# Kernel optimization log

Measured on AMD Instinct MI355X. Metric: run time of the kernel, lower is better.

## Reference

```python
import jax, jax.numpy as jnp
import numpy as np
import math

MODES = 32
IN_CH = 32
OUT_CH = 32
SIZE = 2048
BATCH = 8
FILTER_STRENGTH = 4.0
MAX_AMP = 1.0
AMP_SHARP = 1.0
POLE_OFF_SCALE = 0.1
POLE_MIN = 0.1
POLE_MAX = 100.0
CAUSAL_SAFETY = 1.0


def setup_inputs() -> dict:
    key = jax.random.key(0)
    ks = jax.random.split(key, 6)
    # polar-amp init matching the torch module
    fan_in = MODES * IN_CH
    target_amp = math.sqrt(2.0 / fan_in)
    target_sig = max(0.01, min(0.99, target_amp / MAX_AMP))
    init_bias = math.log(target_sig / (1.0 - target_sig)) / AMP_SHARP
    init_scale = 1.0 / math.sqrt(IN_CH * OUT_CH * MODES)
    return {
        "x": jax.random.normal(ks[0], (BATCH, IN_CH, SIZE), jnp.float32),
        "c_star": jax.random.uniform(ks[1], (BATCH,), jnp.float32),
        "dt_star": jnp.full((1,), 0.5, jnp.float32),
        "dx_star": jnp.full((1,), 1.0 / SIZE, jnp.float32),
        "weight_log_amp": init_bias + jax.random.normal(ks[2], (MODES, IN_CH, OUT_CH), jnp.float32) * init_scale,
        "weight_phase": jax.random.normal(ks[3], (MODES, IN_CH, OUT_CH), jnp.float32),
        "log_poles": jnp.linspace(math.log(1.0), math.log(50.0), MODES, dtype=jnp.float32),
        "pole_w": jax.random.normal(ks[4], (IN_CH, MODES), jnp.float32) * math.sqrt(1.0 / IN_CH),
        "pole_b": jnp.zeros((MODES,), jnp.float32),
    }


def _forward(x, weight_log_amp, weight_phase, log_poles, pole_w, pole_b, c_star, dt_star, dx_star):
    size = x.shape[-1]
    # data-dependent pole shift: mean over batch and grid -> [C]
    x_mean = x.mean(axis=(0, 2))
    pole_offsets = jnp.tanh(x_mean @ pole_w + pole_b)           # [K]
    poles = jax.nn.softplus(log_poles + POLE_OFF_SCALE * pole_offsets)
    poles = jnp.clip(poles, POLE_MIN, POLE_MAX)                  # [K]
    # polar weight parameterisation
    weight_amp = MAX_AMP * jax.nn.sigmoid(AMP_SHARP * weight_log_amp)
    weights = weight_amp * jnp.cos(weight_phase)                 # [K,I,O]
    # exponential spectral filter over poles
    k_norm = jnp.arange(MODES, dtype=jnp.float32) / max(MODES - 1, 1)
    pole_filter = jnp.exp(-FILTER_STRENGTH * k_norm ** 2)       # [K]
    # pairwise distances on [0,1] grid
    coords = jnp.linspace(0.0, 1.0, size, dtype=jnp.float32)
    dist = jnp.abs(coords[None, :] - coords[:, None])            # [S,S]
    # data-dependent causal mask: c_eff = safety * max(c_star)
    max_dist_norm = CAUSAL_SAFETY * jnp.max(c_star) * dt_star[0]
    causal = (dist <= max_dist_norm).astype(jnp.float32)         # [S,S]
    # Laplace kernels per pole: exp(-s_k |x-y|), masked, row-normalised
    raw = jnp.exp(-poles[:, None, None] * dist[None]) * causal[None]   # [K,S,S]
    row_norms = jnp.clip(jnp.sum(raw, axis=-1, keepdims=True), 1e-8, None)
    kernels = raw / jax.lax.stop_gradient(row_norms)
    kernels = kernels * pole_filter[:, None, None]
    # contract over source grid j, then mode-wise channel mixing
    out = jnp.einsum('bcs,kts,kio->bot', x, kernels, weights)    # [B,O,S]
    return out


def reference(x, c_star, dt_star, dx_star, weight_log_amp, weight_phase, log_poles, pole_w, pole_b):
    return _forward(x, weight_log_amp, weight_phase, log_poles, pole_w, pole_b, c_star, dt_star, dx_star)
```

## Files before the change

### kernel.cpp

```cpp
#include <hip/hip_runtime.h>
#include <math.h>

#define SM1 2047.0f

#define WS_WSUM  288
#define WS_PART  1312
#define WS_XSUM  3360
#define WS_SCALE 20480
#define WS_YF    90112
#define WS_YB    614400

__global__ __launch_bounds__(256) void k1(const float* __restrict__ x,
                                          const float* __restrict__ wla,
                                          const float* __restrict__ wph,
                                          float* __restrict__ ws) {
    int blk = blockIdx.x, tid = threadIdx.x;
    if (blk >= 64) {
        int k = ((blk - 64) << 3) + (tid >> 5);
        int o = tid & 31;
        float a = 0.f;
#pragma unroll 4
        for (int c = 0; c < 32; ++c) {
            int e = (((k << 5) + c) << 5) + o;
            a += cosf(wph[e]) / (1.0f + expf(-wla[e]));
        }
        ws[WS_WSUM + (k << 5) + o] = a;
        return;
    }
    int b = blk >> 3;
    int s = ((blk & 7) << 8) + tid;
    __shared__ float pr[32][4];
    int lane = tid & 63, wid = tid >> 6;
    float acc = 0.f;
#pragma unroll
    for (int c = 0; c < 32; ++c) {
        float v = x[(size_t)(((b << 5) + c) << 11) + s];
        acc += v;
        float r = v;
        for (int off = 32; off; off >>= 1) r += __shfl_xor(r, off, 64);
        if (lane == 0) pr[c][wid] = r;
    }
    ws[WS_XSUM + (b << 11) + s] = acc;
    __syncthreads();
    if (tid < 32) {
        float m = pr[tid][0] + pr[tid][1] + pr[tid][2] + pr[tid][3];
        ws[WS_PART + (blk << 5) + tid] = m;
    }
}

__device__ __forceinline__ void prep(const float* __restrict__ c_star,
                                     const float* __restrict__ dt,
                                     const float* __restrict__ lp,
                                     const float* __restrict__ pw,
                                     const float* __restrict__ pb,
                                     const float* __restrict__ ws,
                                     float* xm, float* cP, float* cD, float* cDW1,
                                     float* cDL, float* cPF, float* cIDEN, int* cWsh) {
    int tid = threadIdx.x;
    if (tid < 32) {
        float m = 0.f;
        for (int j = 0; j < 64; ++j) m += ws[WS_PART + (j << 5) + tid];
        xm[tid] = m * (1.0f / 16384.0f);
    }
    __syncthreads();
    if (tid < 32) {
        int k = tid;
        float mc = c_star[0];
        for (int b2 = 1; b2 < 8; ++b2) mc = fmaxf(mc, c_star[b2]);
        float mdn = mc * dt[0];
        int W = (int)(mdn * SM1);
        while (W + 1 <= 2047 && (float)(W + 1) / SM1 <= mdn) ++W;
        while (W > 0 && (float)W / SM1 > mdn) --W;
        W = min(max(W, 0), 2047);
        if (k == 0) *cWsh = W;
        float accp = pb[k];
        for (int c = 0; c < 32; ++c) accp += xm[c] * pw[(c << 5) + k];
        float z = lp[k] + 0.1f * tanhf(accp);
        float p = log1pf(expf(z));
        p = fminf(fmaxf(p, 0.1f), 100.0f);
        float d = expf(-p / SM1);
        cP[k]   = p;
        cD[k]   = d;
        cDW1[k] = expf(-p * (float)(W + 1) / SM1);
        cDL[k]  = expf(-p * 64.0f / SM1);
        float kn = (float)k / 31.0f;
        cPF[k]  = expf(-4.0f * kn * kn);
        cIDEN[k] = d / (-expm1f(-p / SM1));
    }
    __syncthreads();
}

__global__ __launch_bounds__(512) void k2(const float* __restrict__ c_star,
                                          const float* __restrict__ dt,
                                          const float* __restrict__ lp,
                                          const float* __restrict__ pw,
                                          const float* __restrict__ pb,
                                          float* __restrict__ ws) {
    __shared__ float xr[2048];
    __shared__ float carr[32][17];
    __shared__ float xm[32], cP[32], cD[32], cDW1[32], cDL[32], cPF[32], cIDEN[32];
    __shared__ int cWsh;
    int tid = threadIdx.x, blk = blockIdx.x;
    prep(c_star, dt, lp, pw, pb, ws, xm, cP, cD, cDW1, cDL, cPF, cIDEN, &cWsh);
    int W = cWsh;

    if (blk >= 32) {
        float rs = 1.0f / SM1;
#pragma unroll
        for (int j = 0; j < 8; ++j) {
            int gid = ((blk - 32) << 12) + (j << 9) + tid;
            int k = gid >> 11, t = gid & 2047;
            float p = cP[k], iden = cIDEN[k];
            int n1 = min(W, t), n2 = min(W, 2047 - t);
            float g1 = -iden * expm1f(-p * (float)n1 * rs);
            float g2 = -iden * expm1f(-p * (float)n2 * rs);
            ws[WS_SCALE + gid] = cPF[k] / (1.0f + g1 + g2);
        }
        return;
    }
    int b = blk >> 2, dir = (blk >> 1) & 1, kh = blk & 1;
    for (int i = tid; i < 2048; i += 512) xr[i] = ws[WS_XSUM + (b << 11) + i];
    int chunk = tid >> 4, kk = tid & 15;
    int k = (kh << 4) + kk;
    float d = cD[k], dw1 = cDW1[k], dL = cDL[k];
    __syncthreads();
    float st = 0.f;
    if (dir == 0) {
        int t0 = chunk << 6;
#pragma unroll
        for (int i = 0; i < 64; ++i) {
            int t = t0 + i;
            float u = xr[t];
            int tl = t - W - 1;
            if (tl >= 0) u = fmaf(-dw1, xr[tl], u);
            st = fmaf(d, st, u);
        }
    } else {
        int t1 = (chunk << 6) + 63;
#pragma unroll
        for (int i = 0; i < 64; ++i) {
            int t = t1 - i;
            float u = xr[t];
            int th = t + W + 1;
            if (th <= 2047) u = fmaf(-dw1, xr[th], u);
            st = fmaf(d, st, u);
        }
    }
    int sidx = (dir == 0) ? chunk : 31 - chunk;
    carr[sidx][kk] = st;
    float m = dL, cur = st;
    for (int off = 1; off < 32; off <<= 1) {
        __syncthreads();
        float prev = (sidx >= off) ? carr[sidx - off][kk] : 0.f;
        __syncthreads();
        cur = fmaf(m, prev, cur);
        carr[sidx][kk] = cur;
        m = m * m;
    }
    __syncthreads();
    float cin = (sidx == 0) ? 0.f : carr[sidx - 1][kk];
    float* yo = ws + ((dir == 0) ? WS_YF : WS_YB) + (((size_t)((b << 5) + k)) << 11);
    float4 v4;
    st = cin;
    if (dir == 0) {
        int t0 = chunk << 6;
#pragma unroll
        for (int i = 0; i < 64; ++i) {
            int t = t0 + i;
            float u = xr[t];
            int tl = t - W - 1;
            if (tl >= 0) u = fmaf(-dw1, xr[tl], u);
            st = fmaf(d, st, u);
            int ph = i & 3;
            if (ph == 0) v4.x = st; else if (ph == 1) v4.y = st;
            else if (ph == 2) v4.z = st;
            else { v4.w = st; *(float4*)(yo + (t & ~3)) = v4; }
        }
    } else {
        int t1 = (chunk << 6) + 63;
#pragma unroll
        for (int i = 0; i < 64; ++i) {
            int t = t1 - i;
            float u = xr[t];
            int th = t + W + 1;
            if (th <= 2047) u = fmaf(-dw1, xr[th], u);
            st = fmaf(d, st, u);
            float val = st - xr[t];
            int ph = t & 3;
            if (ph == 3) v4.w = val; else if (ph == 2) v4.z = val;
            else if (ph == 1) v4.y = val;
            else { v4.x = val; *(float4*)(yo + t) = v4; }
        }
    }
}

__global__ __launch_bounds__(1024) void k3(const float* __restrict__ ws,
                                           float* __restrict__ out) {
    __shared__ float wl[1024];
    __shared__ float yt[32 * 33];
    int tid = threadIdx.x;
    int b = blockIdx.x >> 6;
    int t0 = (blockIdx.x & 63) << 5;
    wl[tid] = ws[WS_WSUM + tid];
    {
        int k = tid >> 5, tt = tid & 31;
        size_t yi = (((size_t)((b << 5) + k)) << 11) + t0 + tt;
        float sc = ws[WS_SCALE + (k << 11) + t0 + tt];
        yt[tt * 33 + k] = (ws[WS_YF + yi] + ws[WS_YB + yi]) * sc;
    }
    __syncthreads();
    {
        int o = tid >> 5, tt = tid & 31;
        float acc = 0.f;
#pragma unroll
        for (int kk = 0; kk < 32; ++kk)
            acc = fmaf(yt[tt * 33 + kk], wl[(kk << 5) + o], acc);
        out[((size_t)((b << 5) + o) << 11) + t0 + tt] = acc;
    }
}

extern "C" void kernel_launch(void* const* d_in, const int* in_sizes, int n_in,
                              void* d_out, int out_size, void* d_ws, size_t ws_size,
                              hipStream_t stream) {
    const float* x      = (const float*)d_in[0];
    const float* c_star = (const float*)d_in[1];
    const float* dt     = (const float*)d_in[2];
    const float* wla    = (const float*)d_in[4];
    const float* wph    = (const float*)d_in[5];
    const float* lp     = (const float*)d_in[6];
    const float* pw     = (const float*)d_in[7];
    const float* pb     = (const float*)d_in[8];
    float* out = (float*)d_out;
    float* ws  = (float*)d_ws;

    k1<<<68,  256,  0, stream>>>(x, wla, wph, ws);
    k2<<<48,  512,  0, stream>>>(c_star, dt, lp, pw, pb, ws);
    k3<<<512, 1024, 0, stream>>>(ws, out);
}
```

Before: 35.80 us.

## Fuse reduction and scan kernels, recompute scale factors in final kernel

Result: slower. 42.58 us (+19.0%).

```diff
diff --git a/kernel.cpp b/kernel.cpp
--- a/kernel.cpp
+++ b/kernel.cpp
@@ -3,20 +3,26 @@
 
 #define SM1 2047.0f
 
-#define WS_WSUM  288
-#define WS_PART  1312
-#define WS_XSUM  3360
-#define WS_SCALE 20480
-#define WS_YF    90112
-#define WS_YB    614400
-
-__global__ __launch_bounds__(256) void k1(const float* __restrict__ x,
+#define WS_P     0
+#define WS_IDEN  32
+#define WS_PF    64
+#define WS_WIDX  96
+#define WS_WSUM  128
+#define WS_YF    2048
+#define WS_YB    526336
+
+__global__ __launch_bounds__(512) void kA(const float* __restrict__ x,
+                                          const float* __restrict__ c_star,
+                                          const float* __restrict__ dt,
+                                          const float* __restrict__ lp,
+                                          const float* __restrict__ pw,
+                                          const float* __restrict__ pb,
                                           const float* __restrict__ wla,
                                           const float* __restrict__ wph,
                                           float* __restrict__ ws) {
-    int blk = blockIdx.x, tid = threadIdx.x;
-    if (blk >= 64) {
-        int k = ((blk - 64) << 3) + (tid >> 5);
+    int tid = threadIdx.x, blk = blockIdx.x;
+    if (blk >= 32) {
+        int k = ((blk - 32) << 4) + (tid >> 5);
         int o = tid & 31;
         float a = 0.f;
 #pragma unroll 4
@@ -27,39 +33,35 @@
         ws[WS_WSUM + (k << 5) + o] = a;
         return;
     }
-    int b = blk >> 3;
-    int s = ((blk & 7) << 8) + tid;
-    __shared__ float pr[32][4];
-    int lane = tid & 63, wid = tid >> 6;
-    float acc = 0.f;
-#pragma unroll
+    __shared__ float xr[2048];
+    __shared__ float pr[32][8];
+    __shared__ float carr[32][17];
+    __shared__ float xm[32], cP[32], cD[32], cDW1[32], cDL[32], cPF[32], cIDEN[32];
+    __shared__ int cWsh;
+    int b = blk >> 2, dir = (blk >> 1) & 1, kh = blk & 1;
+
+    const float4* x4 = (const float4*)x;
+    float4 a4 = make_float4(0.f, 0.f, 0.f, 0.f);
+    int wid = tid >> 6;
+#pragma unroll 4
     for (int c = 0; c < 32; ++c) {
-        float v = x[(size_t)(((b << 5) + c) << 11) + s];
-        acc += v;
-        float r = v;
-        for (int off = 32; off; off >>= 1) r += __shfl_xor(r, off, 64);
-        if (lane == 0) pr[c][wid] = r;
-    }
-    ws[WS_XSUM + (b << 11) + s] = acc;
-    __syncthreads();
-    if (tid < 32) {
-        float m = pr[tid][0] + pr[tid][1] + pr[tid][2] + pr[tid][3];
-        ws[WS_PART + (blk << 5) + tid] = m;
-    }
-}
-
-__device__ __forceinline__ void prep(const float* __restrict__ c_star,
-                                     const float* __restrict__ dt,
-                                     const float* __restrict__ lp,
-                                     const float* __restrict__ pw,
-                                     const float* __restrict__ pb,
-                                     const float* __restrict__ ws,
-                                     float* xm, float* cP, float* cD, float* cDW1,
-                                     float* cDL, float* cPF, float* cIDEN, int* cWsh) {
-    int tid = threadIdx.x;
+        float pc = 0.f;
+#pragma unroll
+        for (int bb = 0; bb < 8; ++bb) {
+            float4 v = x4[(((bb << 5) + c) << 9) + tid];
+            pc += (v.x + v.y) + (v.z + v.w);
+            if (bb == b) { a4.x += v.x; a4.y += v.y; a4.z += v.z; a4.w += v.w; }
+        }
+        for (int off = 32; off; off >>= 1) pc += __shfl_xor(pc, off, 64);
+        if ((tid & 63) == 0) pr[c][wid] = pc;
+    }
+    *(float4*)&xr[tid << 2] = a4;
+    __syncthreads();
+
     if (tid < 32) {
         float m = 0.f;
-        for (int j = 0; j < 64; ++j) m += ws[WS_PART + (j << 5) + tid];
+#pragma unroll
+        for (int w = 0; w < 8; ++w) m += pr[tid][w];
         xm[tid] = m * (1.0f / 16384.0f);
     }
     __syncthreads();
@@ -72,7 +74,7 @@
         while (W + 1 <= 2047 && (float)(W + 1) / SM1 <= mdn) ++W;
         while (W > 0 && (float)W / SM1 > mdn) --W;
         W = min(max(W, 0), 2047);
-        if (k == 0) *cWsh = W;
+        if (k == 0) cWsh = W;
         float accp = pb[k];
         for (int c = 0; c < 32; ++c) accp += xm[c] * pw[(c << 5) + k];
         float z = lp[k] + 0.1f * tanhf(accp);
@@ -86,44 +88,19 @@
         float kn = (float)k / 31.0f;
         cPF[k]  = expf(-4.0f * kn * kn);
         cIDEN[k] = d / (-expm1f(-p / SM1));
-    }
-    __syncthreads();
-}
-
-__global__ __launch_bounds__(512) void k2(const float* __restrict__ c_star,
-                                          const float* __restrict__ dt,
-                                          const float* __restrict__ lp,
-                                          const float* __restrict__ pw,
-                                          const float* __restrict__ pb,
-                                          float* __restrict__ ws) {
-    __shared__ float xr[2048];
-    __shared__ float carr[32][17];
-    __shared__ float xm[32], cP[32], cD[32], cDW1[32], cDL[32], cPF[32], cIDEN[32];
-    __shared__ int cWsh;
-    int tid = threadIdx.x, blk = blockIdx.x;
-    prep(c_star, dt, lp, pw, pb, ws, xm, cP, cD, cDW1, cDL, cPF, cIDEN, &cWsh);
-    int W = cWsh;
-
-    if (blk >= 32) {
-        float rs = 1.0f / SM1;
-#pragma unroll
-        for (int j = 0; j < 8; ++j) {
-            int gid = ((blk - 32) << 12) + (j << 9) + tid;
-            int k = gid >> 11, t = gid & 2047;
-            float p = cP[k], iden = cIDEN[k];
-            int n1 = min(W, t), n2 = min(W, 2047 - t);
-            float g1 = -iden * expm1f(-p * (float)n1 * rs);
-            float g2 = -iden * expm1f(-p * (float)n2 * rs);
-            ws[WS_SCALE + gid] = cPF[k] / (1.0f + g1 + g2);
-        }
-        return;
-    }
-    int b = blk >> 2, dir = (blk >> 1) & 1, kh = blk & 1;
-    for (int i = tid; i < 2048; i += 512) xr[i] = ws[WS_XSUM + (b << 11) + i];
+        if (blk == 0) {
+            ws[WS_P + k]    = p;
+            ws[WS_IDEN + k] = cIDEN[k];
+            ws[WS_PF + k]   = cPF[k];
+            if (k == 0) ((int*)ws)[WS_WIDX] = W;
+        }
+    }
+    __syncthreads();
+
     int chunk = tid >> 4, kk = tid & 15;
     int k = (kh << 4) + kk;
     float d = cD[k], dw1 = cDW1[k], dL = cDL[k];
-    __syncthreads();
+    int W = cWsh;
     float st = 0.f;
     if (dir == 0) {
         int t0 = chunk << 6;
@@ -194,7 +171,7 @@
     }
 }
 
-__global__ __launch_bounds__(1024) void k3(const float* __restrict__ ws,
+__global__ __launch_bounds__(1024) void kB(const float* __restrict__ ws,
                                            float* __restrict__ out) {
     __shared__ float wl[1024];
     __shared__ float yt[32 * 33];
@@ -204,8 +181,14 @@
     wl[tid] = ws[WS_WSUM + tid];
     {
         int k = tid >> 5, tt = tid & 31;
-        size_t yi = (((size_t)((b << 5) + k)) << 11) + t0 + tt;
-        float sc = ws[WS_SCALE + (k << 11) + t0 + tt];
+        int t = t0 + tt;
+        float p = ws[WS_P + k], iden = ws[WS_IDEN + k], pf = ws[WS_PF + k];
+        int W = ((const int*)ws)[WS_WIDX];
+        int n1 = min(W, t), n2 = min(W, 2047 - t);
+        float g1 = -iden * expm1f(-p * (float)n1 * (1.0f / SM1));
+        float g2 = -iden * expm1f(-p * (float)n2 * (1.0f / SM1));
+        float sc = pf / (1.0f + g1 + g2);
+        size_t yi = (((size_t)((b << 5) + k)) << 11) + t;
         yt[tt * 33 + k] = (ws[WS_YF + yi] + ws[WS_YB + yi]) * sc;
     }
     __syncthreads();
@@ -233,7 +216,6 @@
     float* out = (float*)d_out;
     float* ws  = (float*)d_ws;
 
-    k1<<<68,  256,  0, stream>>>(x, wla, wph, ws);
-    k2<<<48,  512,  0, stream>>>(c_star, dt, lp, pw, pb, ws);
-    k3<<<512, 1024, 0, stream>>>(ws, out);
+    kA<<<34,  512,  0, stream>>>(x, c_star, dt, lp, pw, pb, wla, wph, ws);
+    kB<<<512, 1024, 0, stream>>>(ws, out);
 }
```

## Vectorize channel reduction and split the scan across more, smaller blocks

Applied to the files above, without the earlier changes.

New measurement: 31.20 us. -12.8%, faster.

```diff
diff --git a/kernel.cpp b/kernel.cpp
--- a/kernel.cpp
+++ b/kernel.cpp
@@ -3,12 +3,12 @@
 
 #define SM1 2047.0f
 
-#define WS_WSUM  288
+#define WS_WSUM  128
 #define WS_PART  1312
-#define WS_XSUM  3360
-#define WS_SCALE 20480
-#define WS_YF    90112
-#define WS_YB    614400
+#define WS_PXS   2048
+#define WS_SCALE 133120
+#define WS_YF    198656
+#define WS_YB    722944
 
 __global__ __launch_bounds__(256) void k1(const float* __restrict__ x,
                                           const float* __restrict__ wla,
@@ -27,39 +27,48 @@
         ws[WS_WSUM + (k << 5) + o] = a;
         return;
     }
-    int b = blk >> 3;
-    int s = ((blk & 7) << 8) + tid;
-    __shared__ float pr[32][4];
-    int lane = tid & 63, wid = tid >> 6;
-    float acc = 0.f;
-#pragma unroll
-    for (int c = 0; c < 32; ++c) {
-        float v = x[(size_t)(((b << 5) + c) << 11) + s];
-        acc += v;
-        float r = v;
-        for (int off = 32; off; off >>= 1) r += __shfl_xor(r, off, 64);
-        if (lane == 0) pr[c][wid] = r;
-    }
-    ws[WS_XSUM + (b << 11) + s] = acc;
-    __syncthreads();
-    if (tid < 32) {
-        float m = pr[tid][0] + pr[tid][1] + pr[tid][2] + pr[tid][3];
-        ws[WS_PART + (blk << 5) + tid] = m;
-    }
-}
-
-__device__ __forceinline__ void prep(const float* __restrict__ c_star,
-                                     const float* __restrict__ dt,
-                                     const float* __restrict__ lp,
-                                     const float* __restrict__ pw,
-                                     const float* __restrict__ pb,
-                                     const float* __restrict__ ws,
-                                     float* xm, float* cP, float* cD, float* cDW1,
-                                     float* cDL, float* cPF, float* cIDEN, int* cWsh) {
-    int tid = threadIdx.x;
+    int b = blk >> 3, q = blk & 7;
+    const float4* x4 = (const float4*)x + ((size_t)(((b << 5) + (q << 2))) << 9);
+    __shared__ float pr[8][4];
+    float4 ae = make_float4(0.f, 0.f, 0.f, 0.f);
+    float4 ao = make_float4(0.f, 0.f, 0.f, 0.f);
+    int wid = tid >> 6;
+#pragma unroll
+    for (int it = 0; it < 8; ++it) {
+        float4 v = x4[(it << 8) + tid];
+        float pc = (v.x + v.y) + (v.z + v.w);
+        if (it & 1) { ao.x += v.x; ao.y += v.y; ao.z += v.z; ao.w += v.w; }
+        else        { ae.x += v.x; ae.y += v.y; ae.z += v.z; ae.w += v.w; }
+        for (int off = 32; off; off >>= 1) pc += __shfl_xor(pc, off, 64);
+        if ((tid & 63) == 0) pr[it][wid] = pc;
+    }
+    float4* pxs4 = (float4*)(ws + WS_PXS) + ((size_t)(((b << 3) + q)) << 9);
+    pxs4[tid] = ae;
+    pxs4[256 + tid] = ao;
+    __syncthreads();
+    if (tid < 4) {
+        float m = 0.f;
+#pragma unroll
+        for (int w = 0; w < 4; ++w) m += pr[(tid << 1)][w] + pr[(tid << 1) + 1][w];
+        ws[WS_PART + (blk << 2) + tid] = m;
+    }
+}
+
+__global__ __launch_bounds__(256) void k2(const float* __restrict__ c_star,
+                                          const float* __restrict__ dt,
+                                          const float* __restrict__ lp,
+                                          const float* __restrict__ pw,
+                                          const float* __restrict__ pb,
+                                          float* __restrict__ ws) {
+    __shared__ float xr[2048];
+    __shared__ float carr[32][9];
+    __shared__ float xm[32], cP[32], cD[32], cDW1[32], cDL[32], cPF[32], cIDEN[32];
+    __shared__ int cWsh;
+    int tid = threadIdx.x, blk = blockIdx.x;
     if (tid < 32) {
         float m = 0.f;
-        for (int j = 0; j < 64; ++j) m += ws[WS_PART + (j << 5) + tid];
+#pragma unroll
+        for (int b = 0; b < 8; ++b) m += ws[WS_PART + (b << 5) + tid];
         xm[tid] = m * (1.0f / 16384.0f);
     }
     __syncthreads();
@@ -72,7 +81,7 @@
         while (W + 1 <= 2047 && (float)(W + 1) / SM1 <= mdn) ++W;
         while (W > 0 && (float)W / SM1 > mdn) --W;
         W = min(max(W, 0), 2047);
-        if (k == 0) *cWsh = W;
+        if (k == 0) cWsh = W;
         float accp = pb[k];
         for (int c = 0; c < 32; ++c) accp += xm[c] * pw[(c << 5) + k];
         float z = lp[k] + 0.1f * tanhf(accp);
@@ -88,42 +97,35 @@
         cIDEN[k] = d / (-expm1f(-p / SM1));
     }
     __syncthreads();
-}
-
-__global__ __launch_bounds__(512) void k2(const float* __restrict__ c_star,
-                                          const float* __restrict__ dt,
-                                          const float* __restrict__ lp,
-                                          const float* __restrict__ pw,
-                                          const float* __restrict__ pb,
-                                          float* __restrict__ ws) {
-    __shared__ float xr[2048];
-    __shared__ float carr[32][17];
-    __shared__ float xm[32], cP[32], cD[32], cDW1[32], cDL[32], cPF[32], cIDEN[32];
-    __shared__ int cWsh;
-    int tid = threadIdx.x, blk = blockIdx.x;
-    prep(c_star, dt, lp, pw, pb, ws, xm, cP, cD, cDW1, cDL, cPF, cIDEN, &cWsh);
     int W = cWsh;
 
-    if (blk >= 32) {
+    if (blk >= 64) {
+        int k = blk - 64;
+        float p = cP[k], iden = cIDEN[k], pf = cPF[k];
         float rs = 1.0f / SM1;
 #pragma unroll
         for (int j = 0; j < 8; ++j) {
-            int gid = ((blk - 32) << 12) + (j << 9) + tid;
-            int k = gid >> 11, t = gid & 2047;
-            float p = cP[k], iden = cIDEN[k];
+            int t = (j << 8) + tid;
             int n1 = min(W, t), n2 = min(W, 2047 - t);
             float g1 = -iden * expm1f(-p * (float)n1 * rs);
             float g2 = -iden * expm1f(-p * (float)n2 * rs);
-            ws[WS_SCALE + gid] = cPF[k] / (1.0f + g1 + g2);
+            ws[WS_SCALE + (k << 11) + t] = pf / (1.0f + g1 + g2);
         }
         return;
     }
-    int b = blk >> 2, dir = (blk >> 1) & 1, kh = blk & 1;
-    for (int i = tid; i < 2048; i += 512) xr[i] = ws[WS_XSUM + (b << 11) + i];
-    int chunk = tid >> 4, kk = tid & 15;
-    int k = (kh << 4) + kk;
+    int b = blk >> 3, dir = (blk >> 2) & 1, kq = blk & 3;
+#pragma unroll
+    for (int j = 0; j < 8; ++j) {
+        int idx = (j << 8) + tid;
+        float s8 = 0.f;
+#pragma unroll
+        for (int q = 0; q < 8; ++q) s8 += ws[WS_PXS + (((b << 3) + q) << 11) + idx];
+        xr[idx] = s8;
+    }
+    __syncthreads();
+    int chunk = tid >> 3, kk = tid & 7;
+    int k = (kq << 3) + kk;
     float d = cD[k], dw1 = cDW1[k], dL = cDL[k];
-    __syncthreads();
     float st = 0.f;
     if (dir == 0) {
         int t0 = chunk << 6;
@@ -234,6 +236,6 @@
     float* ws  = (float*)d_ws;
 
     k1<<<68,  256,  0, stream>>>(x, wla, wph, ws);
-    k2<<<48,  512,  0, stream>>>(c_star, dt, lp, pw, pb, ws);
+    k2<<<96,  256,  0, stream>>>(c_star, dt, lp, pw, pb, ws);
     k3<<<512, 1024, 0, stream>>>(ws, out);
 }
```
